# Kernel tuning notes

Measured on AMD Instinct MI355X. Metric: run time of the kernel, lower is better.

## Reference

```python
import jax, jax.numpy as jnp
import numpy as np

N_SAMPLES = 8_000_000
NB_CLASSES = 5


def setup_inputs() -> dict:
    key = jax.random.key(0)
    k1, k2 = jax.random.split(key)
    preds = jax.random.normal(k1, (N_SAMPLES, NB_CLASSES), dtype=jnp.float32)
    true = jax.random.randint(k2, (N_SAMPLES,), 0, NB_CLASSES, dtype=jnp.int32)
    return {"preds": preds, "true": true}


def reference(preds, true):
    N, C = preds.shape
    dt = preds.dtype
    cls = jnp.arange(C, dtype=dt)

    # SoftArgmax1D per row (base_index=0, step_size=1), then round -> hard class
    soft_arg = jax.nn.softmax(preds, axis=1) @ cls            # [N]
    pred_idx = jnp.clip(jnp.round(soft_arg).astype(jnp.int32), 0, C - 1)

    # confusion_matrix[true, pred] += 1 via fused scatter-add on flat index
    flat = true * C + pred_idx                                 # [N]
    conf = jnp.zeros((C * C,), dtype=dt).at[flat].add(1.0).reshape(C, C)

    # quadratic kappa weights: (i-j)^2 / (C-1)^2
    weights = (cls[:, None] - cls[None, :]) ** 2 / ((C - 1) ** 2)

    # class histograms (scatter-add)
    true_hist = jnp.zeros((C,), dtype=dt).at[true].add(1.0)
    pred_hist = jnp.zeros((C,), dtype=dt).at[pred_idx].add(1.0)

    # expected matrix E = outer(true_hist, pred_hist), both normalized
    E = jnp.outer(true_hist, pred_hist)
    E = E / E.sum()
    conf = conf / conf.sum()

    num = (conf * weights).sum()
    den = (E * weights).sum()
    return num / den
```

## Files before the change

### kernel.cpp

```cpp
#include <hip/hip_runtime.h>
#include <math.h>

#define NCLS 5
#define NBINS 25
#define NBLOCKS 512
#define NTHREADS 256

__global__ void __launch_bounds__(NTHREADS)
kappa_count(const float* __restrict__ preds,
            const int* __restrict__ truev,
            int N,
            unsigned int* __restrict__ partials) {
    __shared__ unsigned int s_conf[NBINS];
    const int tid = threadIdx.x;
    if (tid < NBINS) s_conf[tid] = 0u;
    __syncthreads();

    const int nquad = N >> 2;
    const int gstride = gridDim.x * blockDim.x;
    for (int q = blockIdx.x * blockDim.x + tid; q < nquad; q += gstride) {
        const float4* p4 = (const float4*)(preds + (size_t)q * 20u);
        float4 a = p4[0];
        float4 b = p4[1];
        float4 c = p4[2];
        float4 d = p4[3];
        float4 e = p4[4];
        int4 t4 = *(const int4*)(truev + (size_t)q * 4u);

        float rows[4][NCLS] = {
            {a.x, a.y, a.z, a.w, b.x},
            {b.y, b.z, b.w, c.x, c.y},
            {c.z, c.w, d.x, d.y, d.z},
            {d.w, e.x, e.y, e.z, e.w}
        };
        int ts[4] = {t4.x, t4.y, t4.z, t4.w};

        #pragma unroll
        for (int r = 0; r < 4; r++) {
            float m = rows[r][0];
            #pragma unroll
            for (int j = 1; j < NCLS; j++) m = fmaxf(m, rows[r][j]);
            float s = 0.f, dot = 0.f;
            #pragma unroll
            for (int j = 0; j < NCLS; j++) {
                float ex = __expf(rows[r][j] - m);
                s += ex;
                dot += ex * (float)j;
            }
            int pi = (int)rintf(dot / s);
            pi = min(max(pi, 0), NCLS - 1);
            atomicAdd(&s_conf[ts[r] * NCLS + pi], 1u);
        }
    }

    if (blockIdx.x == 0 && tid < (N & 3)) {
        int i = (N & ~3) + tid;
        float v[NCLS];
        #pragma unroll
        for (int j = 0; j < NCLS; j++) v[j] = preds[(size_t)i * NCLS + j];
        float m = v[0];
        #pragma unroll
        for (int j = 1; j < NCLS; j++) m = fmaxf(m, v[j]);
        float s = 0.f, dot = 0.f;
        #pragma unroll
        for (int j = 0; j < NCLS; j++) {
            float ex = __expf(v[j] - m);
            s += ex;
            dot += ex * (float)j;
        }
        int pi = (int)rintf(dot / s);
        pi = min(max(pi, 0), NCLS - 1);
        atomicAdd(&s_conf[truev[i] * NCLS + pi], 1u);
    }

    __syncthreads();
    if (tid < NBINS) partials[blockIdx.x * NBINS + tid] = s_conf[tid];
}

__global__ void kappa_final(const unsigned int* __restrict__ partials,
                            int nblocks,
                            float* __restrict__ out) {
    __shared__ unsigned int s_conf[NBINS];
    const int tid = threadIdx.x;
    if (tid < NBINS) s_conf[tid] = 0u;
    __syncthreads();

    const int total = nblocks * NBINS;
    for (int i = tid; i < total; i += blockDim.x) {
        unsigned int v = partials[i];
        if (v) atomicAdd(&s_conf[i % NBINS], v);
    }
    __syncthreads();

    if (tid == 0) {
        double conf[NBINS];
        double tot = 0.0;
        for (int i = 0; i < NBINS; i++) { conf[i] = (double)s_conf[i]; tot += conf[i]; }
        double th[NCLS] = {0, 0, 0, 0, 0};
        double ph[NCLS] = {0, 0, 0, 0, 0};
        for (int i = 0; i < NCLS; i++)
            for (int j = 0; j < NCLS; j++) {
                th[i] += conf[i * NCLS + j];
                ph[j] += conf[i * NCLS + j];
            }
        double num = 0.0, den = 0.0;
        for (int i = 0; i < NCLS; i++)
            for (int j = 0; j < NCLS; j++) {
                double w = (double)((i - j) * (i - j)) / 16.0;
                num += w * conf[i * NCLS + j];
                den += w * th[i] * ph[j];
            }
        out[0] = (float)(num * tot / den);
    }
}

extern "C" void kernel_launch(void* const* d_in, const int* in_sizes, int n_in,
                              void* d_out, int out_size, void* d_ws, size_t ws_size,
                              hipStream_t stream) {
    const float* preds = (const float*)d_in[0];
    const int* truev = (const int*)d_in[1];
    const int N = in_sizes[1];

    int nblocks = NBLOCKS;
    size_t need = (size_t)nblocks * NBINS * sizeof(unsigned int);
    if (need > ws_size) nblocks = (int)(ws_size / (NBINS * sizeof(unsigned int)));
    unsigned int* partials = (unsigned int*)d_ws;

    kappa_count<<<nblocks, NTHREADS, 0, stream>>>(preds, truev, N, partials);
    kappa_final<<<1, 256, 0, stream>>>(partials, nblocks, (float*)d_out);
}
```

Before: 257.2 us.

## Double-buffer preds through LDS with async global_load_lds and per-wave histograms

Switches the count kernel to chunked processing: each block stages 1024-row chunks of preds into a double-buffered LDS area using direct global-to-LDS loads, prefetching the next chunk while the current one is computed. Each row is then read from LDS with a row-per-thread mapping, and each wave keeps its own histogram copy to cut atomic contention. Grid size goes up to 2048 blocks. The goal is better memory-level parallelism and coalescing, at the cost of more LDS use, explicit waitcnt/barrier synchronization, and LDS bank conflicts from the stride-5 reads.

```diff
diff --git a/kernel.cpp b/kernel.cpp
--- a/kernel.cpp
+++ b/kernel.cpp
@@ -3,78 +3,111 @@
 
 #define NCLS 5
 #define NBINS 25
-#define NBLOCKS 512
 #define NTHREADS 256
+#define NBLOCKS 2048
+#define CHUNK_ROWS 1024
+#define CHUNK_FLOATS (CHUNK_ROWS * NCLS)
+#define CHUNK_F4 (CHUNK_FLOATS / 4)
+#define ISSUES_PER_WAVE 5
+
+__device__ __forceinline__ void gload_lds16(const void* g, void* l) {
+    __builtin_amdgcn_global_load_lds(
+        (const __attribute__((address_space(1))) unsigned int*)(const unsigned int*)g,
+        (__attribute__((address_space(3))) unsigned int*)(unsigned int*)l,
+        16, 0, 0);
+}
 
 __global__ void __launch_bounds__(NTHREADS)
 kappa_count(const float* __restrict__ preds,
             const int* __restrict__ truev,
             int N,
             unsigned int* __restrict__ partials) {
-    __shared__ unsigned int s_conf[NBINS];
+    __shared__ float s_stage[2][CHUNK_FLOATS];
+    __shared__ unsigned int s_conf[4 * 32];
+
     const int tid = threadIdx.x;
-    if (tid < NBINS) s_conf[tid] = 0u;
+    const int wv = tid >> 6;
+    const int lane = tid & 63;
+
+    if (tid < 128) s_conf[tid] = 0u;
     __syncthreads();
 
-    const int nquad = N >> 2;
-    const int gstride = gridDim.x * blockDim.x;
-    for (int q = blockIdx.x * blockDim.x + tid; q < nquad; q += gstride) {
-        const float4* p4 = (const float4*)(preds + (size_t)q * 20u);
-        float4 a = p4[0];
-        float4 b = p4[1];
-        float4 c = p4[2];
-        float4 d = p4[3];
-        float4 e = p4[4];
-        int4 t4 = *(const int4*)(truev + (size_t)q * 4u);
+    const int nchunks = N / CHUNK_ROWS;
+    const int G = gridDim.x;
 
-        float rows[4][NCLS] = {
-            {a.x, a.y, a.z, a.w, b.x},
-            {b.y, b.z, b.w, c.x, c.y},
-            {c.z, c.w, d.x, d.y, d.z},
-            {d.w, e.x, e.y, e.z, e.w}
-        };
-        int ts[4] = {t4.x, t4.y, t4.z, t4.w};
+    auto stage = [&](int c, int b) {
+        const float4* src = (const float4*)preds + (size_t)c * CHUNK_F4;
+        #pragma unroll
+        for (int k = 0; k < ISSUES_PER_WAVE; ++k) {
+            const int seg = wv * ISSUES_PER_WAVE + k;
+            gload_lds16(src + seg * 64 + lane,
+                        &s_stage[b][seg * 256]);
+        }
+    };
 
+    unsigned int* hist = &s_conf[wv << 5];
+
+    int c = (int)blockIdx.x;
+    int cur = 0;
+    if (c < nchunks) stage(c, 0);
+
+    for (; c < nchunks; c += G) {
+        const int cn = c + G;
+        if (cn < nchunks) {
+            stage(cn, cur ^ 1);
+            asm volatile("s_waitcnt vmcnt(5)" ::: "memory");
+        } else {
+            asm volatile("s_waitcnt vmcnt(0)" ::: "memory");
+        }
+        __builtin_amdgcn_s_barrier();
+        asm volatile("" ::: "memory");
+
+        const int rbase = c * CHUNK_ROWS;
+        int ts[4];
         #pragma unroll
-        for (int r = 0; r < 4; r++) {
-            float m = rows[r][0];
-            #pragma unroll
-            for (int j = 1; j < NCLS; j++) m = fmaxf(m, rows[r][j]);
-            float s = 0.f, dot = 0.f;
-            #pragma unroll
-            for (int j = 0; j < NCLS; j++) {
-                float ex = __expf(rows[r][j] - m);
-                s += ex;
-                dot += ex * (float)j;
-            }
+        for (int rr = 0; rr < 4; ++rr) ts[rr] = truev[rbase + tid + (rr << 8)];
+
+        const float* bufp = s_stage[cur];
+        #pragma unroll
+        for (int rr = 0; rr < 4; ++rr) {
+            const float* rp = bufp + (tid + (rr << 8)) * NCLS;
+            float r0 = rp[0], r1 = rp[1], r2 = rp[2], r3 = rp[3], r4 = rp[4];
+            float m = fmaxf(fmaxf(fmaxf(fmaxf(r0, r1), r2), r3), r4);
+            float e0 = __expf(r0 - m), e1 = __expf(r1 - m), e2 = __expf(r2 - m),
+                  e3 = __expf(r3 - m), e4 = __expf(r4 - m);
+            float s = e0 + e1 + e2 + e3 + e4;
+            float dot = e1 + e2 * 2.f + e3 * 3.f + e4 * 4.f;
             int pi = (int)rintf(dot / s);
             pi = min(max(pi, 0), NCLS - 1);
-            atomicAdd(&s_conf[ts[r] * NCLS + pi], 1u);
+            atomicAdd(&hist[ts[rr] * NCLS + pi], 1u);
+        }
+        asm volatile("" ::: "memory");
+        __builtin_amdgcn_s_barrier();
+        cur ^= 1;
+    }
+
+    if (blockIdx.x == 0) {
+        for (int r = nchunks * CHUNK_ROWS + tid; r < N; r += NTHREADS) {
+            float v0 = preds[(size_t)r * NCLS + 0];
+            float v1 = preds[(size_t)r * NCLS + 1];
+            float v2 = preds[(size_t)r * NCLS + 2];
+            float v3 = preds[(size_t)r * NCLS + 3];
+            float v4 = preds[(size_t)r * NCLS + 4];
+            float m = fmaxf(fmaxf(fmaxf(fmaxf(v0, v1), v2), v3), v4);
+            float e0 = __expf(v0 - m), e1 = __expf(v1 - m), e2 = __expf(v2 - m),
+                  e3 = __expf(v3 - m), e4 = __expf(v4 - m);
+            float s = e0 + e1 + e2 + e3 + e4;
+            float dot = e1 + e2 * 2.f + e3 * 3.f + e4 * 4.f;
+            int pi = (int)rintf(dot / s);
+            pi = min(max(pi, 0), NCLS - 1);
+            atomicAdd(&hist[truev[r] * NCLS + pi], 1u);
         }
     }
 
-    if (blockIdx.x == 0 && tid < (N & 3)) {
-        int i = (N & ~3) + tid;
-        float v[NCLS];
-        #pragma unroll
-        for (int j = 0; j < NCLS; j++) v[j] = preds[(size_t)i * NCLS + j];
-        float m = v[0];
-        #pragma unroll
-        for (int j = 1; j < NCLS; j++) m = fmaxf(m, v[j]);
-        float s = 0.f, dot = 0.f;
-        #pragma unroll
-        for (int j = 0; j < NCLS; j++) {
-            float ex = __expf(v[j] - m);
-            s += ex;
-            dot += ex * (float)j;
-        }
-        int pi = (int)rintf(dot / s);
-        pi = min(max(pi, 0), NCLS - 1);
-        atomicAdd(&s_conf[truev[i] * NCLS + pi], 1u);
-    }
-
     __syncthreads();
-    if (tid < NBINS) partials[blockIdx.x * NBINS + tid] = s_conf[tid];
+    if (tid < NBINS)
+        partials[blockIdx.x * NBINS + tid] =
+            s_conf[tid] + s_conf[32 + tid] + s_conf[64 + tid] + s_conf[96 + tid];
 }
 
 __global__ void kappa_final(const unsigned int* __restrict__ partials,
```

After: 301.4 us. 1.17x slower.
